# Performance work log

Hardware: AMD Instinct MI355X
Metric: run time of the kernel (lower is better)

The kernel has to match this reference:

```python
import jax, jax.numpy as jnp
import numpy as np

N_NODES = 100000
N_EDGES = 1600000
F_IN, F_HID, F_OUT = 128, 128, 40


def setup_inputs() -> dict:
    key = jax.random.key(0)
    ks = jax.random.split(key, 8)
    x = jax.random.normal(ks[0], (N_NODES, F_IN), dtype=jnp.float32)
    edge_index = jax.random.randint(ks[1], (2, N_EDGES), 0, N_NODES, dtype=jnp.int64)
    # GCNConv weights (glorot-style scale); biases zero per bias_init=zeros_
    W0 = jax.random.normal(ks[2], (F_IN, F_HID), dtype=jnp.float32) / np.sqrt(F_IN)
    b0 = jnp.zeros((F_HID,), dtype=jnp.float32)
    W1 = jax.random.normal(ks[3], (F_HID, F_HID), dtype=jnp.float32) / np.sqrt(F_HID)
    b1 = jnp.zeros((F_HID,), dtype=jnp.float32)
    W2 = jax.random.normal(ks[4], (F_HID, F_OUT), dtype=jnp.float32) / np.sqrt(F_HID)
    b2 = jnp.zeros((F_OUT,), dtype=jnp.float32)
    return {"x": x, "edge_index": edge_index, "W0": W0, "b0": b0,
            "W1": W1, "b1": b1, "W2": W2, "b2": b2}


def _gcn_conv(h, src, dst, W, b):
    # PyG GCNConv (normalize=False, add_self_loops=False):
    # linear transform, then sum-aggregate source features at destinations.
    h = h @ W                                   # [N, F_out]
    msgs = jnp.take(h, src, axis=0)             # [E, F_out] gather
    agg = jax.ops.segment_sum(msgs, dst, num_segments=N_NODES)  # scatter-add
    return agg + b


def reference(x, edge_index, W0, b0, W1, b1, W2, b2):
    src, dst = edge_index[0], edge_index[1]     # flow: source -> target
    h = jax.nn.relu(_gcn_conv(x, src, dst, W0, b0))
    h = jax.nn.relu(_gcn_conv(h, src, dst, W1, b1))
    out = _gcn_conv(h, src, dst, W2, b2)        # last layer: no activation
    return out
```

## Files before the change

kernel.cpp:

```cpp
#include <hip/hip_runtime.h>


typedef short bf16x8 __attribute__((ext_vector_type(8)));
typedef float f32x4  __attribute__((ext_vector_type(4)));

#define EPB 8192

__device__ __forceinline__ float bflo(unsigned int v) {
  union { float f; unsigned int i; } w; w.i = v << 16; return w.f;
}
__device__ __forceinline__ float bfhi(unsigned int v) {
  union { float f; unsigned int i; } w; w.i = v & 0xffff0000u; return w.f;
}
__device__ __forceinline__ unsigned short f2bf(float f) {
  union { float f; unsigned int i; } w; w.f = f;
  unsigned int b = w.i;
  unsigned int r = (b + 0x7fffu + ((b >> 16) & 1u)) >> 16;
  return (unsigned short)r;
}

__device__ __forceinline__ int edge_at(const void* ei, int is64, long long pos) {
  if (is64) return (int)((const long long*)ei)[pos];
  return ((const int*)ei)[pos];
}

__device__ __forceinline__ int detect64(const void* ei, int* s_is64, int tid) {
  if (tid < 64) {
    int v = ((const int*)ei)[2 * tid + 1];
    unsigned long long m = __ballot(v != 0);
    if (tid == 0) *s_is64 = (m == 0ull) ? 1 : 0;
  }
  __syncthreads();
  return *s_is64;
}

__global__ __launch_bounds__(256) void k_prep(const void* __restrict__ ei, int E,
                                              int* __restrict__ bhist,
                                              int NBKT, int NBLKE,
                                              const float* __restrict__ x,
                                              unsigned short* __restrict__ xb,
                                              long long n4, int ncvt,
                                              const float* __restrict__ W0,
                                              const float* __restrict__ W1,
                                              const float* __restrict__ W2,
                                              unsigned short* __restrict__ Wt0,
                                              unsigned short* __restrict__ Wt1,
                                              unsigned short* __restrict__ Wt2,
                                              int FOUT) {
  int blk = blockIdx.x, tid = threadIdx.x;
  if (blk < NBLKE) {
    __shared__ int h[512];
    __shared__ int s_is64;
    if (tid < 64) {
      int v = ((const int*)ei)[2 * tid + 1];
      unsigned long long m = __ballot(v != 0);
      if (tid == 0) s_is64 = (m == 0ull) ? 1 : 0;
    }
    for (int i = tid; i < NBKT; i += 256) h[i] = 0;
    __syncthreads();
    int is64 = s_is64;
    int base = blk * EPB;
    int cnt = min(EPB, E - base);
    for (int i = tid; i < cnt; i += 256) {
      int d = edge_at(ei, is64, (long long)E + base + i);
      atomicAdd(&h[d >> 8], 1);
    }
    __syncthreads();
    for (int i = tid; i < NBKT; i += 256) bhist[i * NBLKE + blk] = h[i];
  } else if (blk < NBLKE + ncvt) {
    long long i = (long long)(blk - NBLKE) * 256 + tid;
    if (i < n4) {
      float4 v = *reinterpret_cast<const float4*>(x + i * 4);
      ushort4 o;
      o.x = f2bf(v.x); o.y = f2bf(v.y); o.z = f2bf(v.z); o.w = f2bf(v.w);
      *reinterpret_cast<ushort4*>(xb + i * 4) = o;
    }
  } else {
    int idx = (blk - NBLKE - ncvt) * 256 + tid;
    if (idx < 16384) {
      int c = idx >> 7, k = idx & 127;
      Wt0[c * 128 + k] = f2bf(W0[k * 128 + c]);
    } else if (idx < 32768) {
      int t = idx - 16384;
      int c = t >> 7, k = t & 127;
      Wt1[c * 128 + k] = f2bf(W1[k * 128 + c]);
    } else if (idx < 32768 + 8192) {
      int t = idx - 32768;
      int c = t >> 7, k = t & 127;
      Wt2[c * 128 + k] = (c < FOUT) ? f2bf(W2[k * FOUT + c]) : (unsigned short)0;
    }
  }
}

__global__ void k_scan_a(const int* __restrict__ vals, int* __restrict__ lscan,
                         int* __restrict__ partials, int n) {
  __shared__ int sm[256];
  int tid = threadIdx.x;
  int i = blockIdx.x * 256 + tid;
  int v = (i < n) ? vals[i] : 0;
  sm[tid] = v;
  __syncthreads();
  for (int off = 1; off < 256; off <<= 1) {
    int t = (tid >= off) ? sm[tid - off] : 0;
    __syncthreads();
    sm[tid] += t;
    __syncthreads();
  }
  if (i < n) lscan[i] = sm[tid];
  if (tid == 255) partials[blockIdx.x] = sm[255];
}

__global__ void k_scan_b(int* __restrict__ partials, int nb) {
  __shared__ int sm[1024];
  int tid = threadIdx.x;
  int v = (tid < nb) ? partials[tid] : 0;
  sm[tid] = v;
  __syncthreads();
  for (int off = 1; off < 1024; off <<= 1) {
    int t = (tid >= off) ? sm[tid - off] : 0;
    __syncthreads();
    sm[tid] += t;
    __syncthreads();
  }
  if (tid < nb) partials[tid] = sm[tid] - v;
}

__global__ void k_scan_c(const int* __restrict__ lscan, const int* __restrict__ vals,
                         const int* __restrict__ partials, int* __restrict__ scanned,
                         int* __restrict__ bucketPtr, int n, int NBLKE, int NBKT, int E) {
  int i = blockIdx.x * 256 + threadIdx.x;
  if (i >= n) return;
  int v = lscan[i] - vals[i] + partials[blockIdx.x];
  scanned[i] = v;
  int q = i / NBLKE;
  if (i - q * NBLKE == 0) bucketPtr[q] = v;
  if (i == 0) bucketPtr[NBKT] = E;
}

__global__ __launch_bounds__(256) void b_scatter(const void* __restrict__ ei, int E,
                                                 const int* __restrict__ scanned,
                                                 unsigned* __restrict__ ebuf,
                                                 int NBKT, int NBLKE) {
  __shared__ int base[512];
  __shared__ int s_is64;
  int blk = blockIdx.x, tid = threadIdx.x;
  if (tid < 64) {
    int v = ((const int*)ei)[2 * tid + 1];
    unsigned long long m = __ballot(v != 0);
    if (tid == 0) s_is64 = (m == 0ull) ? 1 : 0;
  }
  for (int i = tid; i < NBKT; i += 256) base[i] = scanned[i * NBLKE + blk];
  __syncthreads();
  int is64 = s_is64;
  int b0 = blk * EPB;
  int cnt = min(EPB, E - b0);
  for (int i = tid; i < cnt; i += 256) {
    int d = edge_at(ei, is64, (long long)E + b0 + i);
    int s = edge_at(ei, is64, b0 + i);
    int pos = atomicAdd(&base[d >> 8], 1);
    ebuf[pos] = (unsigned)s | ((unsigned)(d & 255) << 24);
  }
}

__global__ __launch_bounds__(256) void b_pass2(const unsigned* __restrict__ ebuf,
                                               const int* __restrict__ bucketPtr,
                                               int* __restrict__ rowptr,
                                               int* __restrict__ colsrc,
                                               int N, int NBKT, int E) {
  __shared__ int hist[256], excl[256], cur[256], sm[256];
  int b = blockIdx.x, tid = threadIdx.x;
  hist[tid] = 0;
  __syncthreads();
  int beg = bucketPtr[b], end = bucketPtr[b + 1];
  for (int i = beg + tid; i < end; i += 256)
    atomicAdd(&hist[ebuf[i] >> 24], 1);
  __syncthreads();
  int v = hist[tid];
  sm[tid] = v;
  __syncthreads();
  for (int off = 1; off < 256; off <<= 1) {
    int t = (tid >= off) ? sm[tid - off] : 0;
    __syncthreads();
    sm[tid] += t;
    __syncthreads();
  }
  excl[tid] = sm[tid] - v;
  cur[tid] = 0;
  __syncthreads();
  int nb0 = b << 8;
  if (nb0 + tid < N) rowptr[nb0 + tid] = beg + excl[tid];
  if (b == 0 && tid == 0) rowptr[N] = E;
  for (int i = beg + tid; i < end; i += 256) {
    unsigned e2 = ebuf[i];
    int dl = (int)(e2 >> 24);
    int r = atomicAdd(&cur[dl], 1);
    colsrc[beg + excl[dl] + r] = (int)(e2 & 0xFFFFFFu);
  }
}

__global__ void k_agg128b(const unsigned int* __restrict__ H,
                          const int* __restrict__ rowptr, const int* __restrict__ colsrc,
                          unsigned int* __restrict__ out, int N) {
  int node = blockIdx.x * 4 + (threadIdx.x >> 6);
  if (node >= N) return;
  int l = threadIdx.x & 63;
  int sub = l >> 4, fl = l & 15;
  int beg = rowptr[node], end = rowptr[node + 1];
  float a[8] = {0.f, 0.f, 0.f, 0.f, 0.f, 0.f, 0.f, 0.f};
  int i = beg + sub;
  for (; i + 12 < end; i += 16) {
    int s0 = colsrc[i], s1 = colsrc[i + 4], s2 = colsrc[i + 8], s3 = colsrc[i + 12];
    uint4 v0 = *reinterpret_cast<const uint4*>(H + (size_t)s0 * 64 + fl * 4);
    uint4 v1 = *reinterpret_cast<const uint4*>(H + (size_t)s1 * 64 + fl * 4);
    uint4 v2 = *reinterpret_cast<const uint4*>(H + (size_t)s2 * 64 + fl * 4);
    uint4 v3 = *reinterpret_cast<const uint4*>(H + (size_t)s3 * 64 + fl * 4);
    a[0] += (bflo(v0.x) + bflo(v1.x)) + (bflo(v2.x) + bflo(v3.x));
    a[1] += (bfhi(v0.x) + bfhi(v1.x)) + (bfhi(v2.x) + bfhi(v3.x));
    a[2] += (bflo(v0.y) + bflo(v1.y)) + (bflo(v2.y) + bflo(v3.y));
    a[3] += (bfhi(v0.y) + bfhi(v1.y)) + (bfhi(v2.y) + bfhi(v3.y));
    a[4] += (bflo(v0.z) + bflo(v1.z)) + (bflo(v2.z) + bflo(v3.z));
    a[5] += (bfhi(v0.z) + bfhi(v1.z)) + (bfhi(v2.z) + bfhi(v3.z));
    a[6] += (bflo(v0.w) + bflo(v1.w)) + (bflo(v2.w) + bflo(v3.w));
    a[7] += (bfhi(v0.w) + bfhi(v1.w)) + (bfhi(v2.w) + bfhi(v3.w));
  }
  for (; i < end; i += 4) {
    uint4 v = *reinterpret_cast<const uint4*>(H + (size_t)colsrc[i] * 64 + fl * 4);
    a[0] += bflo(v.x); a[1] += bfhi(v.x);
    a[2] += bflo(v.y); a[3] += bfhi(v.y);
    a[4] += bflo(v.z); a[5] += bfhi(v.z);
    a[6] += bflo(v.w); a[7] += bfhi(v.w);
  }
  #pragma unroll
  for (int k = 0; k < 8; ++k) {
    a[k] += __shfl_xor(a[k], 16);
    a[k] += __shfl_xor(a[k], 32);
  }
  if (sub == 0) {
    uint4 o;
    o.x = ((unsigned)f2bf(a[1]) << 16) | f2bf(a[0]);
    o.y = ((unsigned)f2bf(a[3]) << 16) | f2bf(a[2]);
    o.z = ((unsigned)f2bf(a[5]) << 16) | f2bf(a[4]);
    o.w = ((unsigned)f2bf(a[7]) << 16) | f2bf(a[6]);
    *reinterpret_cast<uint4*>(out + (size_t)node * 64 + fl * 4) = o;
  }
}

__global__ void k_agg40(const unsigned int* __restrict__ T,
                        const int* __restrict__ rowptr, const int* __restrict__ colsrc,
                        const float* __restrict__ b2, float* __restrict__ out, int N) {
  int node = blockIdx.x * 4 + (threadIdx.x >> 6);
  if (node >= N) return;
  int l = threadIdx.x & 63;
  int sub = l >> 4, fl = l & 15;
  int beg = rowptr[node], end = rowptr[node + 1];
  float a[4] = {0.f, 0.f, 0.f, 0.f};
  int i = beg + sub;
  for (; i + 12 < end; i += 16) {
    int s0 = colsrc[i], s1 = colsrc[i + 4], s2 = colsrc[i + 8], s3 = colsrc[i + 12];
    uint2 v0 = *reinterpret_cast<const uint2*>(T + (size_t)s0 * 32 + fl * 2);
    uint2 v1 = *reinterpret_cast<const uint2*>(T + (size_t)s1 * 32 + fl * 2);
    uint2 v2 = *reinterpret_cast<const uint2*>(T + (size_t)s2 * 32 + fl * 2);
    uint2 v3 = *reinterpret_cast<const uint2*>(T + (size_t)s3 * 32 + fl * 2);
    a[0] += (bflo(v0.x) + bflo(v1.x)) + (bflo(v2.x) + bflo(v3.x));
    a[1] += (bfhi(v0.x) + bfhi(v1.x)) + (bfhi(v2.x) + bfhi(v3.x));
    a[2] += (bflo(v0.y) + bflo(v1.y)) + (bflo(v2.y) + bflo(v3.y));
    a[3] += (bfhi(v0.y) + bfhi(v1.y)) + (bfhi(v2.y) + bfhi(v3.y));
  }
  for (; i < end; i += 4) {
    uint2 v = *reinterpret_cast<const uint2*>(T + (size_t)colsrc[i] * 32 + fl * 2);
    a[0] += bflo(v.x); a[1] += bfhi(v.x);
    a[2] += bflo(v.y); a[3] += bfhi(v.y);
  }
  #pragma unroll
  for (int k = 0; k < 4; ++k) {
    a[k] += __shfl_xor(a[k], 16);
    a[k] += __shfl_xor(a[k], 32);
  }
  if (sub == 0 && fl < 10) {
    float4 o;
    o.x = a[0] + b2[fl * 4 + 0];
    o.y = a[1] + b2[fl * 4 + 1];
    o.z = a[2] + b2[fl * 4 + 2];
    o.w = a[3] + b2[fl * 4 + 3];
    *reinterpret_cast<float4*>(out + (size_t)node * 40 + fl * 4) = o;
  }
}

template <int CHAIN>
__global__ __launch_bounds__(256) void k_gemm(const unsigned short* __restrict__ A,
                                              const unsigned short* __restrict__ Wt,
                                              const float* __restrict__ bias,
                                              const unsigned short* __restrict__ Wt2,
                                              unsigned short* __restrict__ C, int N) {
  __shared__ unsigned short sh16[CHAIN ? 4 * 2048 : 64];
  int tid = threadIdx.x;
  int w = tid >> 6, l = tid & 63;
  int sub = l >> 4, fl = l & 15;
  int r0 = blockIdx.x * 64 + w * 16;
  int arow = r0 + fl;
  if (arow >= N) arow = N - 1;
  int kk = sub * 8;
  bf16x8 af[4];
  #pragma unroll
  for (int ks = 0; ks < 4; ++ks)
    af[ks] = *reinterpret_cast<const bf16x8*>(A + (size_t)arow * 128 + ks * 32 + kk);

  int ccol = fl;
  int crow0 = r0 + sub * 4;

  if (CHAIN == 0) {
    #pragma unroll
    for (int cf = 0; cf < 8; ++cf) {
      f32x4 acc = {0.f, 0.f, 0.f, 0.f};
      const unsigned short* wp = Wt + (size_t)(cf * 16 + ccol) * 128 + kk;
      #pragma unroll
      for (int ks = 0; ks < 4; ++ks) {
        bf16x8 b = *reinterpret_cast<const bf16x8*>(wp + ks * 32);
        acc = __builtin_amdgcn_mfma_f32_16x16x32_bf16(af[ks], b, acc, 0, 0, 0);
      }
      float bv = bias[cf * 16 + ccol];
      #pragma unroll
      for (int r = 0; r < 4; ++r) {
        int gr = crow0 + r;
        if (gr < N)
          C[(size_t)gr * 128 + cf * 16 + ccol] = f2bf(fmaxf(acc[r] + bv, 0.f));
      }
    }
  } else {
    unsigned short* my = &sh16[w * 2048];
    #pragma unroll
    for (int cf = 0; cf < 8; ++cf) {
      f32x4 acc = {0.f, 0.f, 0.f, 0.f};
      const unsigned short* wp = Wt + (size_t)(cf * 16 + ccol) * 128 + kk;
      #pragma unroll
      for (int ks = 0; ks < 4; ++ks) {
        bf16x8 b = *reinterpret_cast<const bf16x8*>(wp + ks * 32);
        acc = __builtin_amdgcn_mfma_f32_16x16x32_bf16(af[ks], b, acc, 0, 0, 0);
      }
      float bv = bias[cf * 16 + ccol];
      int col = cf * 16 + ccol;
      int chunk = col >> 3;
      #pragma unroll
      for (int r = 0; r < 4; ++r) {
        int row = sub * 4 + r;
        my[row * 128 + ((chunk ^ row) << 3) + (col & 7)] = f2bf(fmaxf(acc[r] + bv, 0.f));
      }
    }
    bf16x8 af3[4];
    #pragma unroll
    for (int ks = 0; ks < 4; ++ks) {
      int c = ks * 4 + sub;
      af3[ks] = *reinterpret_cast<const bf16x8*>(&my[fl * 128 + ((c ^ fl) << 3)]);
    }
    #pragma unroll
    for (int cf = 0; cf < 4; ++cf) {
      f32x4 acc = {0.f, 0.f, 0.f, 0.f};
      const unsigned short* wp = Wt2 + (size_t)(cf * 16 + ccol) * 128 + kk;
      #pragma unroll
      for (int ks = 0; ks < 4; ++ks) {
        bf16x8 b = *reinterpret_cast<const bf16x8*>(wp + ks * 32);
        acc = __builtin_amdgcn_mfma_f32_16x16x32_bf16(af3[ks], b, acc, 0, 0, 0);
      }
      #pragma unroll
      for (int r = 0; r < 4; ++r) {
        int gr = crow0 + r;
        if (gr < N)
          C[(size_t)gr * 64 + cf * 16 + ccol] = f2bf(acc[r]);
      }
    }
  }
}

extern "C" void kernel_launch(void* const* d_in, const int* in_sizes, int n_in,
                              void* d_out, int out_size, void* d_ws, size_t ws_size,
                              hipStream_t stream) {
  const float* x  = (const float*)d_in[0];
  const void*  ei = d_in[1];
  const float* W0 = (const float*)d_in[2];
  const float* b0 = (const float*)d_in[3];
  const float* W1 = (const float*)d_in[4];
  const float* b1 = (const float*)d_in[5];
  const float* W2 = (const float*)d_in[6];
  const float* b2 = (const float*)d_in[7];
  float* out = (float*)d_out;

  const int N = in_sizes[0] / 128;
  const int E = in_sizes[1] / 2;
  const int FOUT = in_sizes[6] / 128;

  const int NBLKE = (E + EPB - 1) / EPB;
  const int NBKT  = (N + 255) / 256;
  const int T     = NBKT * NBLKE;
  const int GS    = (T + 255) / 256;

  char* wp = (char*)d_ws;
  auto alloc = [&](size_t bytes) -> void* {
    void* p = (void*)wp;
    wp += (bytes + 255) & ~(size_t)255;
    return p;
  };
  unsigned short* xb   = (unsigned short*)alloc((size_t)N * 128 * 2);
  unsigned short* bufA = (unsigned short*)alloc((size_t)N * 128 * 2);
  unsigned short* bufH = (unsigned short*)alloc((size_t)N * 128 * 2);
  unsigned short* t3   = (unsigned short*)alloc((size_t)N * 64 * 2);
  unsigned short* Wt0  = (unsigned short*)alloc(128 * 128 * 2);
  unsigned short* Wt1  = (unsigned short*)alloc(128 * 128 * 2);
  unsigned short* Wt2  = (unsigned short*)alloc(64 * 128 * 2);
  unsigned* ebuf = (unsigned*)alloc((size_t)E * 4);
  int* colsrc   = (int*)alloc((size_t)E * 4);
  int* rowptr   = (int*)alloc((size_t)(N + 1) * 4);
  int* bhist    = (int*)alloc((size_t)T * 4);
  int* lscan    = (int*)alloc((size_t)T * 4);
  int* scanned  = (int*)alloc((size_t)T * 4);
  int* partials = (int*)alloc(4096);
  int* bucketPtr= (int*)alloc((size_t)(NBKT + 1) * 4);

  long long n4 = (long long)N * 32;
  int ncvt = (int)((n4 + 255) / 256);
  int nwt  = (32768 + 8192 + 255) / 256;

  k_prep<<<NBLKE + ncvt + nwt, 256, 0, stream>>>(ei, E, bhist, NBKT, NBLKE,
                                                 x, xb, n4, ncvt,
                                                 W0, W1, W2, Wt0, Wt1, Wt2, FOUT);
  k_scan_a<<<GS, 256, 0, stream>>>(bhist, lscan, partials, T);
  k_scan_b<<<1, 1024, 0, stream>>>(partials, GS);
  k_scan_c<<<GS, 256, 0, stream>>>(lscan, bhist, partials, scanned, bucketPtr,
                                   T, NBLKE, NBKT, E);
  b_scatter<<<NBLKE, 256, 0, stream>>>(ei, E, scanned, ebuf, NBKT, NBLKE);
  b_pass2<<<NBKT, 256, 0, stream>>>(ebuf, bucketPtr, rowptr, colsrc, N, NBKT, E);

  int gagg = (N + 3) / 4;
  int ggemm = (N + 63) / 64;
  k_agg128b<<<gagg, 256, 0, stream>>>((const unsigned int*)xb, rowptr, colsrc,
                                      (unsigned int*)bufA, N);
  k_gemm<0><<<ggemm, 256, 0, stream>>>(bufA, Wt0, b0, nullptr, bufH, N);
  k_agg128b<<<gagg, 256, 0, stream>>>((const unsigned int*)bufH, rowptr, colsrc,
                                      (unsigned int*)bufA, N);
  k_gemm<1><<<ggemm, 256, 0, stream>>>(bufA, Wt1, b1, Wt2, t3, N);
  k_agg40<<<gagg, 256, 0, stream>>>((const unsigned int*)t3, rowptr, colsrc,
                                    b2, out, N);
}
```

Before: 305.4 us.

## Fuse aggregation with MFMA GEMM per node group; pad with zero row for branchless gathers

Each aggregation kernel now feeds straight into the following dense GEMM inside one kernel. A block aggregates 4 nodes into shared memory, then runs MFMA against the weight matrix, so the intermediate bufA round trip through global memory and two kernel launches go away. The neighbour loops are made branchless: out-of-range edges read an extra zero row appended to each feature buffer and cleared in the prep kernel. The cost is that each block computes only 4 rows of MFMA output, so every block reloads the full weight tile from cache. Padded slots issue wasted loads, and the 40-wide kernel now idles 6 of 16 lanes.

```diff
diff --git a/kernel.cpp b/kernel.cpp
--- a/kernel.cpp
+++ b/kernel.cpp
@@ -24,14 +24,11 @@
   return ((const int*)ei)[pos];
 }
 
-__device__ __forceinline__ int detect64(const void* ei, int* s_is64, int tid) {
-  if (tid < 64) {
-    int v = ((const int*)ei)[2 * tid + 1];
-    unsigned long long m = __ballot(v != 0);
-    if (tid == 0) *s_is64 = (m == 0ull) ? 1 : 0;
-  }
-  __syncthreads();
-  return *s_is64;
+__device__ __forceinline__ void agg_accum(float* a, uint4 v) {
+  a[0] += bflo(v.x); a[1] += bfhi(v.x);
+  a[2] += bflo(v.y); a[3] += bfhi(v.y);
+  a[4] += bflo(v.z); a[5] += bfhi(v.z);
+  a[6] += bflo(v.w); a[7] += bfhi(v.w);
 }
 
 __global__ __launch_bounds__(256) void k_prep(const void* __restrict__ ei, int E,
@@ -46,7 +43,9 @@
                                               unsigned short* __restrict__ Wt0,
                                               unsigned short* __restrict__ Wt1,
                                               unsigned short* __restrict__ Wt2,
-                                              int FOUT) {
+                                              unsigned short* __restrict__ bufH,
+                                              unsigned short* __restrict__ t3,
+                                              int FOUT, int N) {
   int blk = blockIdx.x, tid = threadIdx.x;
   if (blk < NBLKE) {
     __shared__ int h[512];
@@ -84,10 +83,15 @@
       int t = idx - 16384;
       int c = t >> 7, k = t & 127;
       Wt1[c * 128 + k] = f2bf(W1[k * 128 + c]);
-    } else if (idx < 32768 + 8192) {
+    } else if (idx < 40960) {
       int t = idx - 32768;
       int c = t >> 7, k = t & 127;
       Wt2[c * 128 + k] = (c < FOUT) ? f2bf(W2[k * FOUT + c]) : (unsigned short)0;
+    } else if (idx < 41280) {
+      int t = idx - 40960;
+      if (t < 128)       xb[(size_t)N * 128 + t] = 0;
+      else if (t < 256)  bufH[(size_t)N * 128 + (t - 128)] = 0;
+      else               t3[(size_t)N * 64 + (t - 256)] = 0;
     }
   }
 }
@@ -198,37 +202,42 @@
   }
 }
 
-__global__ void k_agg128b(const unsigned int* __restrict__ H,
-                          const int* __restrict__ rowptr, const int* __restrict__ colsrc,
-                          unsigned int* __restrict__ out, int N) {
-  int node = blockIdx.x * 4 + (threadIdx.x >> 6);
-  if (node >= N) return;
-  int l = threadIdx.x & 63;
-  int sub = l >> 4, fl = l & 15;
-  int beg = rowptr[node], end = rowptr[node + 1];
+template <int CHAIN>
+__global__ __launch_bounds__(256, 6) void k_fused(
+    const char* __restrict__ Hb, const int* __restrict__ rowptr,
+    const int* __restrict__ colsrc,
+    const unsigned short* __restrict__ Wt, const float* __restrict__ bias,
+    const unsigned short* __restrict__ Wt2, unsigned short* __restrict__ C,
+    int N) {
+  __shared__ unsigned int aggT[256];
+  __shared__ unsigned int outT[256];
+  int tid = threadIdx.x, w = tid >> 6, l = tid & 63, sub = l >> 4, fl = l & 15;
+  int node = blockIdx.x * 4 + w;
+  int nc = (node < N) ? node : (N - 1);
+  int beg = rowptr[nc], end = rowptr[nc + 1];
+  int cnt = end - beg;
+  int nb = (cnt + 15) >> 4;
+  const unsigned zoff = (unsigned)N << 8;
+  unsigned flo = (unsigned)fl * 16u;
   float a[8] = {0.f, 0.f, 0.f, 0.f, 0.f, 0.f, 0.f, 0.f};
-  int i = beg + sub;
-  for (; i + 12 < end; i += 16) {
-    int s0 = colsrc[i], s1 = colsrc[i + 4], s2 = colsrc[i + 8], s3 = colsrc[i + 12];
-    uint4 v0 = *reinterpret_cast<const uint4*>(H + (size_t)s0 * 64 + fl * 4);
-    uint4 v1 = *reinterpret_cast<const uint4*>(H + (size_t)s1 * 64 + fl * 4);
-    uint4 v2 = *reinterpret_cast<const uint4*>(H + (size_t)s2 * 64 + fl * 4);
-    uint4 v3 = *reinterpret_cast<const uint4*>(H + (size_t)s3 * 64 + fl * 4);
-    a[0] += (bflo(v0.x) + bflo(v1.x)) + (bflo(v2.x) + bflo(v3.x));
-    a[1] += (bfhi(v0.x) + bfhi(v1.x)) + (bfhi(v2.x) + bfhi(v3.x));
-    a[2] += (bflo(v0.y) + bflo(v1.y)) + (bflo(v2.y) + bflo(v3.y));
-    a[3] += (bfhi(v0.y) + bfhi(v1.y)) + (bfhi(v2.y) + bfhi(v3.y));
-    a[4] += (bflo(v0.z) + bflo(v1.z)) + (bflo(v2.z) + bflo(v3.z));
-    a[5] += (bfhi(v0.z) + bfhi(v1.z)) + (bfhi(v2.z) + bfhi(v3.z));
-    a[6] += (bflo(v0.w) + bflo(v1.w)) + (bflo(v2.w) + bflo(v3.w));
-    a[7] += (bfhi(v0.w) + bfhi(v1.w)) + (bfhi(v2.w) + bfhi(v3.w));
-  }
-  for (; i < end; i += 4) {
-    uint4 v = *reinterpret_cast<const uint4*>(H + (size_t)colsrc[i] * 64 + fl * 4);
-    a[0] += bflo(v.x); a[1] += bfhi(v.x);
-    a[2] += bflo(v.y); a[3] += bfhi(v.y);
-    a[4] += bflo(v.z); a[5] += bfhi(v.z);
-    a[6] += bflo(v.w); a[7] += bfhi(v.w);
+
+  for (int t = 0; t < nb; ++t) {
+    int e = beg + t * 16 + sub * 4;
+    int em = end - 1;
+    int i0 = e, i1 = e + 1, i2 = e + 2, i3 = e + 3;
+    int s0 = colsrc[i0 < end ? i0 : em];
+    int s1 = colsrc[i1 < end ? i1 : em];
+    int s2 = colsrc[i2 < end ? i2 : em];
+    int s3 = colsrc[i3 < end ? i3 : em];
+    unsigned o0 = (i0 < end ? ((unsigned)s0 << 8) : zoff) + flo;
+    unsigned o1 = (i1 < end ? ((unsigned)s1 << 8) : zoff) + flo;
+    unsigned o2 = (i2 < end ? ((unsigned)s2 << 8) : zoff) + flo;
+    unsigned o3 = (i3 < end ? ((unsigned)s3 << 8) : zoff) + flo;
+    uint4 v0 = *reinterpret_cast<const uint4*>(Hb + o0);
+    uint4 v1 = *reinterpret_cast<const uint4*>(Hb + o1);
+    uint4 v2 = *reinterpret_cast<const uint4*>(Hb + o2);
+    uint4 v3 = *reinterpret_cast<const uint4*>(Hb + o3);
+    agg_accum(a, v0); agg_accum(a, v1); agg_accum(a, v2); agg_accum(a, v3);
   }
   #pragma unroll
   for (int k = 0; k < 8; ++k) {
@@ -241,35 +250,98 @@
     o.y = ((unsigned)f2bf(a[3]) << 16) | f2bf(a[2]);
     o.z = ((unsigned)f2bf(a[5]) << 16) | f2bf(a[4]);
     o.w = ((unsigned)f2bf(a[7]) << 16) | f2bf(a[6]);
-    *reinterpret_cast<uint4*>(out + (size_t)node * 64 + fl * 4) = o;
-  }
-}
-
-__global__ void k_agg40(const unsigned int* __restrict__ T,
-                        const int* __restrict__ rowptr, const int* __restrict__ colsrc,
-                        const float* __restrict__ b2, float* __restrict__ out, int N) {
+    *reinterpret_cast<uint4*>(&aggT[w * 64 + fl * 4]) = o;
+  }
+  __syncthreads();
+
+  int r4 = l & 3;
+  bf16x8 af[4];
+  #pragma unroll
+  for (int ks = 0; ks < 4; ++ks)
+    af[ks] = *reinterpret_cast<const bf16x8*>(&aggT[r4 * 64 + (ks * 4 + sub) * 4]);
+
+  unsigned short* outS = (unsigned short*)outT;
+  #pragma unroll
+  for (int q = 0; q < 2; ++q) {
+    int cf = w * 2 + q;
+    f32x4 acc = {0.f, 0.f, 0.f, 0.f};
+    const unsigned short* wp = Wt + (size_t)(cf * 16 + fl) * 128 + sub * 8;
+    #pragma unroll
+    for (int ks = 0; ks < 4; ++ks) {
+      bf16x8 b = *reinterpret_cast<const bf16x8*>(wp + ks * 32);
+      acc = __builtin_amdgcn_mfma_f32_16x16x32_bf16(af[ks], b, acc, 0, 0, 0);
+    }
+    float bv = bias[cf * 16 + fl];
+    if (sub == 0) {
+      #pragma unroll
+      for (int r = 0; r < 4; ++r)
+        outS[r * 128 + cf * 16 + fl] = f2bf(fmaxf(acc[r] + bv, 0.f));
+    }
+  }
+  __syncthreads();
+
+  if (CHAIN == 0) {
+    if (node < N)
+      ((unsigned int*)C)[(size_t)node * 64 + l] = outT[w * 64 + l];
+  } else {
+    bf16x8 af3[4];
+    #pragma unroll
+    for (int ks = 0; ks < 4; ++ks)
+      af3[ks] = *reinterpret_cast<const bf16x8*>(&outT[r4 * 64 + (ks * 4 + sub) * 4]);
+    f32x4 acc = {0.f, 0.f, 0.f, 0.f};
+    const unsigned short* wp = Wt2 + (size_t)(w * 16 + fl) * 128 + sub * 8;
+    #pragma unroll
+    for (int ks = 0; ks < 4; ++ks) {
+      bf16x8 b = *reinterpret_cast<const bf16x8*>(wp + ks * 32);
+      acc = __builtin_amdgcn_mfma_f32_16x16x32_bf16(af3[ks], b, acc, 0, 0, 0);
+    }
+    unsigned short* stg = (unsigned short*)aggT;
+    if (sub == 0) {
+      #pragma unroll
+      for (int r = 0; r < 4; ++r)
+        stg[r * 64 + w * 16 + fl] = f2bf(acc[r]);
+    }
+    __syncthreads();
+    if (node < N && l < 32)
+      ((unsigned int*)C)[(size_t)node * 32 + l] = aggT[w * 32 + l];
+  }
+}
+
+__global__ __launch_bounds__(256, 6) void k_agg40(
+    const char* __restrict__ Tb, const int* __restrict__ rowptr,
+    const int* __restrict__ colsrc, const float* __restrict__ b2,
+    float* __restrict__ out, int N) {
   int node = blockIdx.x * 4 + (threadIdx.x >> 6);
   if (node >= N) return;
-  int l = threadIdx.x & 63;
-  int sub = l >> 4, fl = l & 15;
+  int l = threadIdx.x & 63, sub = l >> 4, fl = l & 15;
   int beg = rowptr[node], end = rowptr[node + 1];
+  int cnt = end - beg;
+  int nb = (cnt + 15) >> 4;
+  const unsigned zoff = (unsigned)N << 7;
+  unsigned flo = (unsigned)fl * 8u;
   float a[4] = {0.f, 0.f, 0.f, 0.f};
-  int i = beg + sub;
-  for (; i + 12 < end; i += 16) {
-    int s0 = colsrc[i], s1 = colsrc[i + 4], s2 = colsrc[i + 8], s3 = colsrc[i + 12];
-    uint2 v0 = *reinterpret_cast<const uint2*>(T + (size_t)s0 * 32 + fl * 2);
-    uint2 v1 = *reinterpret_cast<const uint2*>(T + (size_t)s1 * 32 + fl * 2);
-    uint2 v2 = *reinterpret_cast<const uint2*>(T + (size_t)s2 * 32 + fl * 2);
-    uint2 v3 = *reinterpret_cast<const uint2*>(T + (size_t)s3 * 32 + fl * 2);
-    a[0] += (bflo(v0.x) + bflo(v1.x)) + (bflo(v2.x) + bflo(v3.x));
-    a[1] += (bfhi(v0.x) + bfhi(v1.x)) + (bfhi(v2.x) + bfhi(v3.x));
-    a[2] += (bflo(v0.y) + bflo(v1.y)) + (bflo(v2.y) + bflo(v3.y));
-    a[3] += (bfhi(v0.y) + bfhi(v1.y)) + (bfhi(v2.y) + bfhi(v3.y));
-  }
-  for (; i < end; i += 4) {
-    uint2 v = *reinterpret_cast<const uint2*>(T + (size_t)colsrc[i] * 32 + fl * 2);
-    a[0] += bflo(v.x); a[1] += bfhi(v.x);
-    a[2] += bflo(v.y); a[3] += bfhi(v.y);
+  if (fl < 10) {
+    for (int t = 0; t < nb; ++t) {
+      int e = beg + t * 16 + sub * 4;
+      int em = end - 1;
+      int i0 = e, i1 = e + 1, i2 = e + 2, i3 = e + 3;
+      int s0 = colsrc[i0 < end ? i0 : em];
+      int s1 = colsrc[i1 < end ? i1 : em];
+      int s2 = colsrc[i2 < end ? i2 : em];
+      int s3 = colsrc[i3 < end ? i3 : em];
+      unsigned o0 = (i0 < end ? ((unsigned)s0 << 7) : zoff) + flo;
+      unsigned o1 = (i1 < end ? ((unsigned)s1 << 7) : zoff) + flo;
+      unsigned o2 = (i2 < end ? ((unsigned)s2 << 7) : zoff) + flo;
+      unsigned o3 = (i3 < end ? ((unsigned)s3 << 7) : zoff) + flo;
+      uint2 v0 = *reinterpret_cast<const uint2*>(Tb + o0);
+      uint2 v1 = *reinterpret_cast<const uint2*>(Tb + o1);
+      uint2 v2 = *reinterpret_cast<const uint2*>(Tb + o2);
+      uint2 v3 = *reinterpret_cast<const uint2*>(Tb + o3);
+      a[0] += (bflo(v0.x) + bflo(v1.x)) + (bflo(v2.x) + bflo(v3.x));
+      a[1] += (bfhi(v0.x) + bfhi(v1.x)) + (bfhi(v2.x) + bfhi(v3.x));
+      a[2] += (bflo(v0.y) + bflo(v1.y)) + (bflo(v2.y) + bflo(v3.y));
+      a[3] += (bfhi(v0.y) + bfhi(v1.y)) + (bfhi(v2.y) + bfhi(v3.y));
+    }
   }
   #pragma unroll
   for (int k = 0; k < 4; ++k) {
@@ -283,91 +355,6 @@
     o.z = a[2] + b2[fl * 4 + 2];
     o.w = a[3] + b2[fl * 4 + 3];
     *reinterpret_cast<float4*>(out + (size_t)node * 40 + fl * 4) = o;
-  }
-}
-
-template <int CHAIN>
-__global__ __launch_bounds__(256) void k_gemm(const unsigned short* __restrict__ A,
-                                              const unsigned short* __restrict__ Wt,
-                                              const float* __restrict__ bias,
-                                              const unsigned short* __restrict__ Wt2,
-                                              unsigned short* __restrict__ C, int N) {
-  __shared__ unsigned short sh16[CHAIN ? 4 * 2048 : 64];
-  int tid = threadIdx.x;
-  int w = tid >> 6, l = tid & 63;
-  int sub = l >> 4, fl = l & 15;
-  int r0 = blockIdx.x * 64 + w * 16;
-  int arow = r0 + fl;
-  if (arow >= N) arow = N - 1;
-  int kk = sub * 8;
-  bf16x8 af[4];
-  #pragma unroll
-  for (int ks = 0; ks < 4; ++ks)
-    af[ks] = *reinterpret_cast<const bf16x8*>(A + (size_t)arow * 128 + ks * 32 + kk);
-
-  int ccol = fl;
-  int crow0 = r0 + sub * 4;
-
-  if (CHAIN == 0) {
-    #pragma unroll
-    for (int cf = 0; cf < 8; ++cf) {
-      f32x4 acc = {0.f, 0.f, 0.f, 0.f};
-      const unsigned short* wp = Wt + (size_t)(cf * 16 + ccol) * 128 + kk;
-      #pragma unroll
-      for (int ks = 0; ks < 4; ++ks) {
-        bf16x8 b = *reinterpret_cast<const bf16x8*>(wp + ks * 32);
-        acc = __builtin_amdgcn_mfma_f32_16x16x32_bf16(af[ks], b, acc, 0, 0, 0);
-      }
-      float bv = bias[cf * 16 + ccol];
-      #pragma unroll
-      for (int r = 0; r < 4; ++r) {
-        int gr = crow0 + r;
-        if (gr < N)
-          C[(size_t)gr * 128 + cf * 16 + ccol] = f2bf(fmaxf(acc[r] + bv, 0.f));
-      }
-    }
-  } else {
-    unsigned short* my = &sh16[w * 2048];
-    #pragma unroll
-    for (int cf = 0; cf < 8; ++cf) {
-      f32x4 acc = {0.f, 0.f, 0.f, 0.f};
-      const unsigned short* wp = Wt + (size_t)(cf * 16 + ccol) * 128 + kk;
-      #pragma unroll
-      for (int ks = 0; ks < 4; ++ks) {
-        bf16x8 b = *reinterpret_cast<const bf16x8*>(wp + ks * 32);
-        acc = __builtin_amdgcn_mfma_f32_16x16x32_bf16(af[ks], b, acc, 0, 0, 0);
-      }
-      float bv = bias[cf * 16 + ccol];
-      int col = cf * 16 + ccol;
-      int chunk = col >> 3;
-      #pragma unroll
-      for (int r = 0; r < 4; ++r) {
-        int row = sub * 4 + r;
-        my[row * 128 + ((chunk ^ row) << 3) + (col & 7)] = f2bf(fmaxf(acc[r] + bv, 0.f));
-      }
-    }
-    bf16x8 af3[4];
-    #pragma unroll
-    for (int ks = 0; ks < 4; ++ks) {
-      int c = ks * 4 + sub;
-      af3[ks] = *reinterpret_cast<const bf16x8*>(&my[fl * 128 + ((c ^ fl) << 3)]);
-    }
-    #pragma unroll
-    for (int cf = 0; cf < 4; ++cf) {
-      f32x4 acc = {0.f, 0.f, 0.f, 0.f};
-      const unsigned short* wp = Wt2 + (size_t)(cf * 16 + ccol) * 128 + kk;
-      #pragma unroll
-      for (int ks = 0; ks < 4; ++ks) {
-        bf16x8 b = *reinterpret_cast<const bf16x8*>(wp + ks * 32);
-        acc = __builtin_amdgcn_mfma_f32_16x16x32_bf16(af3[ks], b, acc, 0, 0, 0);
-      }
-      #pragma unroll
-      for (int r = 0; r < 4; ++r) {
-        int gr = crow0 + r;
-        if (gr < N)
-          C[(size_t)gr * 64 + cf * 16 + ccol] = f2bf(acc[r]);
-      }
-    }
   }
 }
 
@@ -399,10 +386,9 @@
     wp += (bytes + 255) & ~(size_t)255;
     return p;
   };
-  unsigned short* xb   = (unsigned short*)alloc((size_t)N * 128 * 2);
-  unsigned short* bufA = (unsigned short*)alloc((size_t)N * 128 * 2);
-  unsigned short* bufH = (unsigned short*)alloc((size_t)N * 128 * 2);
-  unsigned short* t3   = (unsigned short*)alloc((size_t)N * 64 * 2);
+  unsigned short* xb   = (unsigned short*)alloc((size_t)(N + 1) * 128 * 2);
+  unsigned short* bufH = (unsigned short*)alloc((size_t)(N + 1) * 128 * 2);
+  unsigned short* t3   = (unsigned short*)alloc((size_t)(N + 1) * 64 * 2);
   unsigned short* Wt0  = (unsigned short*)alloc(128 * 128 * 2);
   unsigned short* Wt1  = (unsigned short*)alloc(128 * 128 * 2);
   unsigned short* Wt2  = (unsigned short*)alloc(64 * 128 * 2);
@@ -417,11 +403,12 @@
 
   long long n4 = (long long)N * 32;
   int ncvt = (int)((n4 + 255) / 256);
-  int nwt  = (32768 + 8192 + 255) / 256;
+  int nwt  = (40960 + 320 + 255) / 256;
 
   k_prep<<<NBLKE + ncvt + nwt, 256, 0, stream>>>(ei, E, bhist, NBKT, NBLKE,
                                                  x, xb, n4, ncvt,
-                                                 W0, W1, W2, Wt0, Wt1, Wt2, FOUT);
+                                                 W0, W1, W2, Wt0, Wt1, Wt2,
+                                                 bufH, t3, FOUT, N);
   k_scan_a<<<GS, 256, 0, stream>>>(bhist, lscan, partials, T);
   k_scan_b<<<1, 1024, 0, stream>>>(partials, GS);
   k_scan_c<<<GS, 256, 0, stream>>>(lscan, bhist, partials, scanned, bucketPtr,
@@ -429,14 +416,10 @@
   b_scatter<<<NBLKE, 256, 0, stream>>>(ei, E, scanned, ebuf, NBKT, NBLKE);
   b_pass2<<<NBKT, 256, 0, stream>>>(ebuf, bucketPtr, rowptr, colsrc, N, NBKT, E);
 
-  int gagg = (N + 3) / 4;
-  int ggemm = (N + 63) / 64;
-  k_agg128b<<<gagg, 256, 0, stream>>>((const unsigned int*)xb, rowptr, colsrc,
-                                      (unsigned int*)bufA, N);
-  k_gemm<0><<<ggemm, 256, 0, stream>>>(bufA, Wt0, b0, nullptr, bufH, N);
-  k_agg128b<<<gagg, 256, 0, stream>>>((const unsigned int*)bufH, rowptr, colsrc,
-                                      (unsigned int*)bufA, N);
-  k_gemm<1><<<ggemm, 256, 0, stream>>>(bufA, Wt1, b1, Wt2, t3, N);
-  k_agg40<<<gagg, 256, 0, stream>>>((const unsigned int*)t3, rowptr, colsrc,
-                                    b2, out, N);
-}
+  int gfuse = (N + 3) / 4;
+  k_fused<0><<<gfuse, 256, 0, stream>>>((const char*)xb, rowptr, colsrc,
+                                        Wt0, b0, nullptr, bufH, N);
+  k_fused<1><<<gfuse, 256, 0, stream>>>((const char*)bufH, rowptr, colsrc,
+                                        Wt1, b1, Wt2, t3, N);
+  k_agg40<<<gfuse, 256, 0, stream>>>((const char*)t3, rowptr, colsrc, b2, out, N);
+}
```

After: 386.8 us. +26.6%, slower.
